# Kernel optimization log

Measured on AMD Instinct MI355X. Metric: run time of the kernel, lower is better.

Reference implementation:

```python
import jax, jax.numpy as jnp
import numpy as np

B, S, E, H = 2, 2048, 1024, 16
D = E // H  # head dim = 64
ROPE_BASE = 10000.0


def _rope(x):
    # x: [B, H, S, D]; interleaved-pair rotary embeddings (torchtune style)
    d2 = D // 2
    theta = 1.0 / (ROPE_BASE ** (jnp.arange(d2, dtype=jnp.float32) * 2.0 / D))  # [D/2]
    pos = jnp.arange(S, dtype=jnp.float32)
    ang = pos[:, None] * theta[None, :]            # [S, D/2]
    cos, sin = jnp.cos(ang), jnp.sin(ang)          # broadcast over B,H
    xr = x.reshape(B, H, S, d2, 2)
    x1, x2 = xr[..., 0], xr[..., 1]
    o1 = x1 * cos - x2 * sin
    o2 = x1 * sin + x2 * cos
    return jnp.stack([o1, o2], axis=-1).reshape(B, H, S, D)


def setup_inputs() -> dict:
    key = jax.random.key(0)
    ks = jax.random.split(key, 5)
    scale = 1.0 / np.sqrt(E)
    return {
        "x": jax.random.normal(ks[0], (B, S, E), dtype=jnp.float32),
        "Wq": jax.random.normal(ks[1], (E, E), dtype=jnp.float32) * scale,
        "Wk": jax.random.normal(ks[2], (E, E), dtype=jnp.float32) * scale,
        "Wv": jax.random.normal(ks[3], (E, E), dtype=jnp.float32) * scale,
        "Wo": jax.random.normal(ks[4], (E, E), dtype=jnp.float32) * scale,
    }


def reference(x, Wq, Wk, Wv, Wo):
    # torch Linear: y = x @ W^T
    def proj(W):
        return (x @ W.T).reshape(B, S, H, D).transpose(0, 2, 1, 3)  # [B,H,S,D]

    q = _rope(proj(Wq))
    k = _rope(proj(Wk))
    v = proj(Wv)

    attn_scale = 1.0 / np.sqrt(E)  # faithful: scales by sqrt(d_embed), not head dim
    scores = jnp.einsum('bhqd,bhkd->bhqk', q, k) * attn_scale  # [B,H,S,S]
    causal = jnp.tril(jnp.ones((S, S), dtype=bool))
    scores = jnp.where(causal, scores, -jnp.inf)
    probs = jax.nn.softmax(scores, axis=-1)
    out = jnp.einsum('bhqk,bhkd->bhqd', probs, v)  # [B,H,S,D]
    out = out.transpose(0, 2, 1, 3).reshape(B, S, E)
    return out @ Wo.T
```

## Files before the change

### kernel.cpp

```cpp
#include <hip/hip_runtime.h>
#include <hip/hip_bf16.h>
#include <math.h>

typedef __bf16 bf16;
typedef __bf16 bf16x8 __attribute__((ext_vector_type(8)));
typedef float f32x4 __attribute__((ext_vector_type(4)));

#define SEQ 2048
#define EMB 1024
#define NH  16
#define HD  64
#define NROWS 4096

#define GLOAD_LDS16(gp, lp)                                             \
    __builtin_amdgcn_global_load_lds(                                   \
        (const __attribute__((address_space(1))) void*)(gp),            \
        (__attribute__((address_space(3))) void*)(lp), 16, 0, 0)

__global__ __launch_bounds__(256) void cvt_rope_kernel(
    const float* __restrict__ x,  const float* __restrict__ Wq,
    const float* __restrict__ Wk, const float* __restrict__ Wv,
    const float* __restrict__ Wo,
    bf16* __restrict__ xb, bf16* __restrict__ Wqb, bf16* __restrict__ Wkb,
    bf16* __restrict__ Wvb, bf16* __restrict__ Wob,
    float* __restrict__ ctab, float* __restrict__ stab)
{
    int b = blockIdx.x;
    if (b >= 4096) {
        int t = (b - 4096) * 256 + threadIdx.x;
        int s = t >> 5;
        int j = t & 31;
        double freq = pow(10000.0, -(double)j / 32.0);
        double ang = (double)s * freq;
        ctab[t] = (float)cos(ang);
        stab[t] = (float)sin(ang);
        return;
    }
    const float* src; bf16* dst; int boff;
    if      (b < 2048) { src = x;  dst = xb;  boff = b;        }
    else if (b < 2560) { src = Wq; dst = Wqb; boff = b - 2048; }
    else if (b < 3072) { src = Wk; dst = Wkb; boff = b - 2560; }
    else if (b < 3584) { src = Wv; dst = Wvb; boff = b - 3072; }
    else               { src = Wo; dst = Wob; boff = b - 3584; }
    size_t off = (size_t)boff * 2048 + (size_t)threadIdx.x * 8;
    float4 f0 = *(const float4*)(src + off);
    float4 f1 = *(const float4*)(src + off + 4);
    bf16x8 v;
    v[0] = (bf16)f0.x; v[1] = (bf16)f0.y; v[2] = (bf16)f0.z; v[3] = (bf16)f0.w;
    v[4] = (bf16)f1.x; v[5] = (bf16)f1.y; v[6] = (bf16)f1.z; v[7] = (bf16)f1.w;
    *(bf16x8*)(dst + off) = v;
}

__global__ __launch_bounds__(256) void qkv_rope_kernel(
    const bf16* __restrict__ x,
    const bf16* __restrict__ Wq, const bf16* __restrict__ Wk, const bf16* __restrict__ Wv,
    const float* __restrict__ ctab, const float* __restrict__ stab,
    bf16* __restrict__ q_ws, bf16* __restrict__ kf_ws, bf16* __restrict__ vf_ws)
{
    __shared__ __align__(16) bf16 SMEM[18432];
    bf16* As = SMEM;
    bf16* Bs = SMEM + 4096;

    const int t    = threadIdx.x;
    const int lane = t & 63;
    const int wave = t >> 6;
    const int col  = lane & 15;
    const int quad = lane >> 4;

    const int nblk = blockIdx.x;
    const int m0   = blockIdx.y * 128;

    const bf16* W; int nloc;
    if (nblk < 8)       { W = Wq; nloc = nblk * 128; }
    else if (nblk < 16) { W = Wk; nloc = (nblk - 8) * 128; }
    else                { W = Wv; nloc = (nblk - 16) * 128; }

    const bf16 *ga[2], *gb[2];
#pragma unroll
    for (int j = 0; j < 2; j++) {
        int c = t + j * 256;
        ga[j] = x + (size_t)(m0 + (c >> 2)) * EMB + (c & 3) * 8;
        gb[j] = W + (size_t)(nloc + (c >> 2)) * EMB + (c & 3) * 8;
    }

    const int wm = (wave >> 1) * 64;
    const int wn = (wave & 1) * 64;

    f32x4 acc[4][4];
#pragma unroll
    for (int i = 0; i < 4; i++)
#pragma unroll
        for (int j = 0; j < 4; j++) acc[i][j] = (f32x4){0.f, 0.f, 0.f, 0.f};

    for (int kc = 0; kc < EMB; kc += 32) {
#pragma unroll
        for (int j = 0; j < 2; j++) {
            int c = t + j * 256;
            GLOAD_LDS16(ga[j] + kc, As + c * 8);
            GLOAD_LDS16(gb[j] + kc, Bs + c * 8);
        }
        __syncthreads();
        bf16x8 a[4], b[4];
#pragma unroll
        for (int mt = 0; mt < 4; mt++)
            a[mt] = *(const bf16x8*)(As + (wm + mt * 16 + col) * 32 + quad * 8);
#pragma unroll
        for (int nt = 0; nt < 4; nt++)
            b[nt] = *(const bf16x8*)(Bs + (wn + nt * 16 + col) * 32 + quad * 8);
#pragma unroll
        for (int mt = 0; mt < 4; mt++)
#pragma unroll
            for (int nt = 0; nt < 4; nt++)
                acc[mt][nt] = __builtin_amdgcn_mfma_f32_16x16x32_bf16(a[mt], b[nt], acc[mt][nt], 0, 0, 0);
        __syncthreads();
    }

    bf16* Es = SMEM + wave * 4608;

    const int n0w  = nblk * 128 + wn;
    const int m0w  = m0 + wm;
    const int bb_  = m0w >> 11;
    const int ss0  = m0w & (SEQ - 1);
    const int h    = (n0w >> 6) & 15;
    const int bh   = bb_ * NH + h;
    const int kind = (n0w < 1024) ? 0 : (n0w < 2048 ? 1 : 2);

#pragma unroll
    for (int mt = 0; mt < 4; mt++) {
#pragma unroll
        for (int nt = 0; nt < 4; nt++) {
            const int d  = nt * 16 + col;
            const int jj = d >> 1;
#pragma unroll
            for (int r = 0; r < 4; r++) {
                const int ss_l = mt * 16 + quad * 4 + r;
                float v = acc[mt][nt][r];
                if (kind < 2) {
                    float partner = __shfl_xor(v, 1, 64);
                    float c  = ctab[(ss0 + ss_l) * 32 + jj];
                    float sn = stab[(ss0 + ss_l) * 32 + jj];
                    float o = ((d & 1) == 0) ? (v * c - partner * sn)
                                             : (partner * sn + v * c);
                    if (kind == 0) {
                        Es[ss_l * 72 + d] = (bf16)(o * 0.03125f);
                    } else {
                        int eoff = ((ss_l >> 4) * 2 + (d >> 5)) * 512
                                 + ((d >> 3) & 3) * 128 + (ss_l & 15) * 8 + (d & 7);
                        Es[eoff] = (bf16)o;
                    }
                } else {
                    int eoff = ((ss_l >> 5) * 4 + (d >> 4)) * 512
                             + ((ss_l >> 3) & 3) * 128 + (d & 15) * 8 + (ss_l & 7);
                    Es[eoff] = (bf16)v;
                }
            }
        }
    }

    const int row = lane >> 3, c8 = lane & 7;
    if (kind == 0) {
        bf16* qbase = q_ws + ((size_t)bh * SEQ + ss0) * HD;
#pragma unroll
        for (int i = 0; i < 8; i++) {
            bf16x8 vv = *(const bf16x8*)&Es[(i * 8 + row) * 72 + c8 * 8];
            *(bf16x8*)(qbase + (size_t)(i * 8 + row) * HD + c8 * 8) = vv;
        }
    } else if (kind == 1) {
        bf16* kbase = kf_ws + ((size_t)bh * 128 + (ss0 >> 4)) * 1024;
#pragma unroll
        for (int i = 0; i < 8; i++) {
            bf16x8 vv = *(const bf16x8*)&Es[i * 512 + lane * 8];
            *(bf16x8*)(kbase + i * 512 + lane * 8) = vv;
        }
    } else {
        bf16* vbase = vf_ws + ((size_t)bh * 64 + (ss0 >> 5)) * 2048;
#pragma unroll
        for (int i = 0; i < 8; i++) {
            bf16x8 vv = *(const bf16x8*)&Es[i * 512 + lane * 8];
            *(bf16x8*)(vbase + i * 512 + lane * 8) = vv;
        }
    }
}

__global__ __launch_bounds__(128) void attn_kernel(
    const bf16* __restrict__ q_ws, const bf16* __restrict__ kf,
    const bf16* __restrict__ vf, bf16* __restrict__ attn_ws)
{
    __shared__ float comb_o[2][4][4][64];
    __shared__ float comb_l[2][64];

    const int lane = threadIdx.x & 63;
    const int wave = threadIdx.x >> 6;
    const int col  = lane & 15;
    const int quad = lane >> 4;

    const int qt = 63 - (int)(blockIdx.x >> 5);
    const int bh = blockIdx.x & 31;
    const int b_ = bh >> 4;
    const int h  = bh & 15;
    const int qb = qt * 32;
    const int nk = qt + 1;

    const bf16* Q  = q_ws + (size_t)bh * SEQ * HD;
    const bf16* Kf = kf + (size_t)bh * 131072;
    const bf16* Vf = vf + (size_t)bh * 131072;

    bf16x8 aq[2][2];
#pragma unroll
    for (int f = 0; f < 2; f++) {
        const bf16* qp = Q + (size_t)(qb + f * 16 + col) * HD + quad * 8;
        aq[f][0] = *(const bf16x8*)(qp);
        aq[f][1] = *(const bf16x8*)(qp + 32);
    }

    f32x4 acc_o[2][4];
#pragma unroll
    for (int f = 0; f < 2; f++)
#pragma unroll
        for (int i = 0; i < 4; i++) acc_o[f][i] = (f32x4){0.f, 0.f, 0.f, 0.f};
    float lsum[2] = {0.f, 0.f};

    int psrc[8];
#pragma unroll
    for (int j = 0; j < 8; j++)
        psrc[j] = ((((quad * 2 + (j >> 2)) & 3) << 4) | col) << 2;

    int s0 = (wave < nk) ? wave : 0;
    bf16x8 Ka[2][2], nKa[2][2];
    {
        const bf16* p = Kf + (size_t)s0 * 2048 + lane * 8;
        Ka[0][0] = *(const bf16x8*)(p);
        Ka[0][1] = *(const bf16x8*)(p + 512);
        Ka[1][0] = *(const bf16x8*)(p + 1024);
        Ka[1][1] = *(const bf16x8*)(p + 1536);
    }

    for (int s = wave; s < nk; s += 2) {
        bf16x8 Vb[4];
        {
            const bf16* p = Vf + (size_t)s * 2048 + lane * 8;
            Vb[0] = *(const bf16x8*)(p);
            Vb[1] = *(const bf16x8*)(p + 512);
            Vb[2] = *(const bf16x8*)(p + 1024);
            Vb[3] = *(const bf16x8*)(p + 1536);
        }

        f32x4 sT[2][2];
#pragma unroll
        for (int g = 0; g < 2; g++)
#pragma unroll
            for (int f = 0; f < 2; f++) {
                f32x4 z = (f32x4){0.f, 0.f, 0.f, 0.f};
                z = __builtin_amdgcn_mfma_f32_16x16x32_bf16(Ka[g][0], aq[f][0], z, 0, 0, 0);
                z = __builtin_amdgcn_mfma_f32_16x16x32_bf16(Ka[g][1], aq[f][1], z, 0, 0, 0);
                sT[g][f] = z;
            }

        {
            int sn = (s + 2 < nk) ? s + 2 : s;
            const bf16* p = Kf + (size_t)sn * 2048 + lane * 8;
            nKa[0][0] = *(const bf16x8*)(p);
            nKa[0][1] = *(const bf16x8*)(p + 512);
            nKa[1][0] = *(const bf16x8*)(p + 1024);
            nKa[1][1] = *(const bf16x8*)(p + 1536);
        }

        float p[2][2][4];
        if (s == nk - 1) {
#pragma unroll
            for (int g = 0; g < 2; g++)
#pragma unroll
                for (int f = 0; f < 2; f++) {
                    const int qg = qb + f * 16 + col;
#pragma unroll
                    for (int r = 0; r < 4; r++) {
                        int key = s * 32 + g * 16 + quad * 4 + r;
                        float e = (key <= qg) ? __expf(sT[g][f][r]) : 0.f;
                        p[g][f][r] = e;
                        lsum[f] += e;
                    }
                }
        } else {
#pragma unroll
            for (int g = 0; g < 2; g++)
#pragma unroll
                for (int f = 0; f < 2; f++)
#pragma unroll
                    for (int r = 0; r < 4; r++) {
                        float e = __expf(sT[g][f][r]);
                        p[g][f][r] = e;
                        lsum[f] += e;
                    }
        }

#pragma unroll
        for (int f = 0; f < 2; f++) {
            unsigned int pk[4];
#pragma unroll
            for (int r = 0; r < 4; r++) {
                unsigned int lo = __builtin_bit_cast(unsigned short, (bf16)p[0][f][r]);
                unsigned int hi = __builtin_bit_cast(unsigned short, (bf16)p[1][f][r]);
                pk[r] = (hi << 16) | lo;
            }
            bf16x8 a_p;
#pragma unroll
            for (int j = 0; j < 8; j++) {
                unsigned int g = (unsigned int)__builtin_amdgcn_ds_bpermute(psrc[j], (int)pk[j & 3]);
                unsigned short bits = (quad < 2) ? (unsigned short)(g & 0xffff)
                                                 : (unsigned short)(g >> 16);
                a_p[j] = __builtin_bit_cast(bf16, bits);
            }
#pragma unroll
            for (int nt = 0; nt < 4; nt++)
                acc_o[f][nt] = __builtin_amdgcn_mfma_f32_16x16x32_bf16(a_p, Vb[nt], acc_o[f][nt], 0, 0, 0);
        }

        Ka[0][0] = nKa[0][0]; Ka[0][1] = nKa[0][1];
        Ka[1][0] = nKa[1][0]; Ka[1][1] = nKa[1][1];
    }

    if (wave == 1) {
#pragma unroll
        for (int f = 0; f < 2; f++) {
            comb_l[f][lane] = lsum[f];
#pragma unroll
            for (int nt = 0; nt < 4; nt++)
#pragma unroll
                for (int r = 0; r < 4; r++)
                    comb_o[f][nt][r][lane] = acc_o[f][nt][r];
        }
    }
    __syncthreads();

    if (wave == 0) {
#pragma unroll
        for (int f = 0; f < 2; f++) {
            lsum[f] += comb_l[f][lane];
#pragma unroll
            for (int nt = 0; nt < 4; nt++)
#pragma unroll
                for (int r = 0; r < 4; r++)
                    acc_o[f][nt][r] += comb_o[f][nt][r][lane];
        }

#pragma unroll
        for (int f = 0; f < 2; f++) {
            lsum[f] += __shfl_xor(lsum[f], 16, 64);
            lsum[f] += __shfl_xor(lsum[f], 32, 64);
        }
#pragma unroll
        for (int f = 0; f < 2; f++)
#pragma unroll
            for (int r = 0; r < 4; r++) {
                float l_r = __shfl(lsum[f], quad * 4 + r, 64);
                float inv = 1.0f / l_r;
                int q = qb + f * 16 + quad * 4 + r;
                bf16* orow = attn_ws + (size_t)(b_ * SEQ + q) * EMB + h * HD;
#pragma unroll
                for (int nt = 0; nt < 4; nt++)
                    orow[nt * 16 + col] = (bf16)(acc_o[f][nt][r] * inv);
            }
    }
}

__global__ __launch_bounds__(256) void oproj_kernel(
    const bf16* __restrict__ attn_ws, const bf16* __restrict__ Wo,
    float* __restrict__ out)
{
    __shared__ __align__(16) char SM[36864];
    bf16* As = (bf16*)SM;
    bf16* Bs = (bf16*)(SM + 8192);

    const int t    = threadIdx.x;
    const int lane = t & 63;
    const int wave = t >> 6;
    const int col  = lane & 15;
    const int quad = lane >> 4;

    const int n0 = blockIdx.x * 64;
    const int m0 = blockIdx.y * 128;

    const bf16 *ga[2], *gb;
#pragma unroll
    for (int j = 0; j < 2; j++) {
        int c = t + j * 256;
        ga[j] = attn_ws + (size_t)(m0 + (c >> 2)) * EMB + (c & 3) * 8;
    }
    gb = Wo + (size_t)(n0 + (t >> 2)) * EMB + (t & 3) * 8;

    const int wm = (wave >> 1) * 64;
    const int wn = (wave & 1) * 32;

    f32x4 acc[4][2];
#pragma unroll
    for (int i = 0; i < 4; i++)
#pragma unroll
        for (int j = 0; j < 2; j++) acc[i][j] = (f32x4){0.f, 0.f, 0.f, 0.f};

    for (int kc = 0; kc < EMB; kc += 32) {
#pragma unroll
        for (int j = 0; j < 2; j++) {
            int c = t + j * 256;
            GLOAD_LDS16(ga[j] + kc, As + c * 8);
        }
        GLOAD_LDS16(gb + kc, Bs + t * 8);
        __syncthreads();
        bf16x8 a[4], b[2];
#pragma unroll
        for (int mt = 0; mt < 4; mt++)
            a[mt] = *(const bf16x8*)(As + (wm + mt * 16 + col) * 32 + quad * 8);
#pragma unroll
        for (int nt = 0; nt < 2; nt++)
            b[nt] = *(const bf16x8*)(Bs + (wn + nt * 16 + col) * 32 + quad * 8);
#pragma unroll
        for (int mt = 0; mt < 4; mt++)
#pragma unroll
            for (int nt = 0; nt < 2; nt++)
                acc[mt][nt] = __builtin_amdgcn_mfma_f32_16x16x32_bf16(a[mt], b[nt], acc[mt][nt], 0, 0, 0);
        __syncthreads();
    }

    float* Os = (float*)(SM + (size_t)wave * 9216);
#pragma unroll
    for (int mt = 0; mt < 4; mt++)
#pragma unroll
        for (int nt = 0; nt < 2; nt++)
#pragma unroll
            for (int r = 0; r < 4; r++)
                Os[(mt * 16 + quad * 4 + r) * 36 + nt * 16 + col] = acc[mt][nt][r];

    const int row = lane >> 3, c8 = lane & 7;
    float* obase = out + (size_t)(m0 + wm) * EMB + n0 + wn;
#pragma unroll
    for (int i = 0; i < 8; i++) {
        float4 vv = *(const float4*)&Os[(i * 8 + row) * 36 + c8 * 4];
        *(float4*)(obase + (size_t)(i * 8 + row) * EMB + c8 * 4) = vv;
    }
}

extern "C" void kernel_launch(void* const* d_in, const int* in_sizes, int n_in,
                              void* d_out, int out_size, void* d_ws, size_t ws_size,
                              hipStream_t stream) {
    const float* x  = (const float*)d_in[0];
    const float* Wq = (const float*)d_in[1];
    const float* Wk = (const float*)d_in[2];
    const float* Wv = (const float*)d_in[3];
    const float* Wo = (const float*)d_in[4];
    float* out = (float*)d_out;

    char* ws = (char*)d_ws;
    bf16* q_ws    = (bf16*)(ws);
    bf16* kf_ws   = (bf16*)(ws + (8u  << 20));
    bf16* vf_ws   = (bf16*)(ws + (16u << 20));
    bf16* xb      = (bf16*)(ws + (24u << 20));
    bf16* attn_ws = (bf16*)(ws + (24u << 20));
    bf16* Wqb     = (bf16*)(ws + (32u << 20));
    bf16* Wkb     = (bf16*)(ws + (34u << 20));
    bf16* Wvb     = (bf16*)(ws + (36u << 20));
    bf16* Wob     = (bf16*)(ws + (38u << 20));
    float* ctab   = (float*)(ws + (40u << 20));
    float* stab   = ctab + SEQ * 32;

    hipLaunchKernelGGL(cvt_rope_kernel, dim3(4352), dim3(256), 0, stream,
                       x, Wq, Wk, Wv, Wo, xb, Wqb, Wkb, Wvb, Wob, ctab, stab);
    hipLaunchKernelGGL(qkv_rope_kernel, dim3(24, 32), dim3(256), 0, stream,
                       xb, Wqb, Wkb, Wvb, ctab, stab, q_ws, kf_ws, vf_ws);
    hipLaunchKernelGGL(attn_kernel, dim3(2048), dim3(128), 0, stream,
                       q_ws, kf_ws, vf_ws, attn_ws);
    hipLaunchKernelGGL(oproj_kernel, dim3(16, 32), dim3(256), 0, stream,
                       attn_ws, Wob, out);
}
```

Baseline: 182.1 us.

## Triple-buffer LDS tiles in QKV and output projection GEMMs with async prefetch

Replaces the load-sync-compute-sync loop in the QKV projection and output projection GEMMs with a three-stage LDS ring buffer. Tiles are prefetched two k-steps ahead with global_load_lds, and a single s_waitcnt vmcnt plus s_barrier per iteration replaces the two __syncthreads. The aim is to hide global-memory latency behind MFMA work and halve barrier count. In exchange it uses more LDS per block in the QKV kernel, which may lower occupancy, and it relies on hand-tuned vmcnt values.

```diff
diff --git a/kernel.cpp b/kernel.cpp
--- a/kernel.cpp
+++ b/kernel.cpp
@@ -57,9 +57,7 @@
     const float* __restrict__ ctab, const float* __restrict__ stab,
     bf16* __restrict__ q_ws, bf16* __restrict__ kf_ws, bf16* __restrict__ vf_ws)
 {
-    __shared__ __align__(16) bf16 SMEM[18432];
-    bf16* As = SMEM;
-    bf16* Bs = SMEM + 4096;
+    __shared__ __align__(16) bf16 SMEM[24576];
 
     const int t    = threadIdx.x;
     const int lane = t & 63;
@@ -92,28 +90,46 @@
 #pragma unroll
         for (int j = 0; j < 4; j++) acc[i][j] = (f32x4){0.f, 0.f, 0.f, 0.f};
 
-    for (int kc = 0; kc < EMB; kc += 32) {
+    auto stage = [&](int kt, int b) {
+        bf16* As_ = SMEM + b * 8192;
+        bf16* Bs_ = As_ + 4096;
+        const int kc = kt * 32;
 #pragma unroll
         for (int j = 0; j < 2; j++) {
-            int c = t + j * 256;
-            GLOAD_LDS16(ga[j] + kc, As + c * 8);
-            GLOAD_LDS16(gb[j] + kc, Bs + c * 8);
-        }
-        __syncthreads();
-        bf16x8 a[4], b[4];
+            const int c = t + j * 256;
+            GLOAD_LDS16(ga[j] + kc, As_ + c * 8);
+            GLOAD_LDS16(gb[j] + kc, Bs_ + c * 8);
+        }
+    };
+    auto compute = [&](int b) {
+        bf16* As_ = SMEM + b * 8192;
+        bf16* Bs_ = As_ + 4096;
+        bf16x8 a[4], bb[4];
 #pragma unroll
         for (int mt = 0; mt < 4; mt++)
-            a[mt] = *(const bf16x8*)(As + (wm + mt * 16 + col) * 32 + quad * 8);
+            a[mt] = *(const bf16x8*)(As_ + (wm + mt * 16 + col) * 32 + quad * 8);
 #pragma unroll
         for (int nt = 0; nt < 4; nt++)
-            b[nt] = *(const bf16x8*)(Bs + (wn + nt * 16 + col) * 32 + quad * 8);
+            bb[nt] = *(const bf16x8*)(Bs_ + (wn + nt * 16 + col) * 32 + quad * 8);
 #pragma unroll
         for (int mt = 0; mt < 4; mt++)
 #pragma unroll
             for (int nt = 0; nt < 4; nt++)
-                acc[mt][nt] = __builtin_amdgcn_mfma_f32_16x16x32_bf16(a[mt], b[nt], acc[mt][nt], 0, 0, 0);
-        __syncthreads();
-    }
+                acc[mt][nt] = __builtin_amdgcn_mfma_f32_16x16x32_bf16(a[mt], bb[nt], acc[mt][nt], 0, 0, 0);
+    };
+
+    stage(0, 0);
+    stage(1, 1);
+    int b = 0;
+    for (int kt = 0; kt < 31; kt++) {
+        asm volatile("s_waitcnt vmcnt(4)\n\ts_barrier" ::: "memory");
+        if (kt < 30) stage(kt + 2, (kt + 2) % 3);
+        compute(b);
+        b = (b == 2) ? 0 : b + 1;
+    }
+    asm volatile("s_waitcnt vmcnt(0)\n\ts_barrier" ::: "memory");
+    compute(b);
+    __syncthreads();
 
     bf16* Es = SMEM + wave * 4608;
 
@@ -368,8 +384,6 @@
     float* __restrict__ out)
 {
     __shared__ __align__(16) char SM[36864];
-    bf16* As = (bf16*)SM;
-    bf16* Bs = (bf16*)(SM + 8192);
 
     const int t    = threadIdx.x;
     const int lane = t & 63;
@@ -397,28 +411,46 @@
 #pragma unroll
         for (int j = 0; j < 2; j++) acc[i][j] = (f32x4){0.f, 0.f, 0.f, 0.f};
 
-    for (int kc = 0; kc < EMB; kc += 32) {
+    auto stage = [&](int kt, int b) {
+        bf16* As_ = (bf16*)(SM + b * 12288);
+        bf16* Bs_ = (bf16*)(SM + b * 12288 + 8192);
+        const int kc = kt * 32;
 #pragma unroll
         for (int j = 0; j < 2; j++) {
-            int c = t + j * 256;
-            GLOAD_LDS16(ga[j] + kc, As + c * 8);
-        }
-        GLOAD_LDS16(gb + kc, Bs + t * 8);
-        __syncthreads();
-        bf16x8 a[4], b[2];
+            const int c = t + j * 256;
+            GLOAD_LDS16(ga[j] + kc, As_ + c * 8);
+        }
+        GLOAD_LDS16(gb + kc, Bs_ + t * 8);
+    };
+    auto compute = [&](int b) {
+        bf16* As_ = (bf16*)(SM + b * 12288);
+        bf16* Bs_ = (bf16*)(SM + b * 12288 + 8192);
+        bf16x8 a[4], bb[2];
 #pragma unroll
         for (int mt = 0; mt < 4; mt++)
-            a[mt] = *(const bf16x8*)(As + (wm + mt * 16 + col) * 32 + quad * 8);
+            a[mt] = *(const bf16x8*)(As_ + (wm + mt * 16 + col) * 32 + quad * 8);
 #pragma unroll
         for (int nt = 0; nt < 2; nt++)
-            b[nt] = *(const bf16x8*)(Bs + (wn + nt * 16 + col) * 32 + quad * 8);
+            bb[nt] = *(const bf16x8*)(Bs_ + (wn + nt * 16 + col) * 32 + quad * 8);
 #pragma unroll
         for (int mt = 0; mt < 4; mt++)
 #pragma unroll
             for (int nt = 0; nt < 2; nt++)
-                acc[mt][nt] = __builtin_amdgcn_mfma_f32_16x16x32_bf16(a[mt], b[nt], acc[mt][nt], 0, 0, 0);
-        __syncthreads();
-    }
+                acc[mt][nt] = __builtin_amdgcn_mfma_f32_16x16x32_bf16(a[mt], bb[nt], acc[mt][nt], 0, 0, 0);
+    };
+
+    stage(0, 0);
+    stage(1, 1);
+    int b = 0;
+    for (int kt = 0; kt < 31; kt++) {
+        asm volatile("s_waitcnt vmcnt(3)\n\ts_barrier" ::: "memory");
+        if (kt < 30) stage(kt + 2, (kt + 2) % 3);
+        compute(b);
+        b = (b == 2) ? 0 : b + 1;
+    }
+    asm volatile("s_waitcnt vmcnt(0)\n\ts_barrier" ::: "memory");
+    compute(b);
+    __syncthreads();
 
     float* Os = (float*)(SM + (size_t)wave * 9216);
 #pragma unroll
```

After: 175.6 us. 1.04x faster.
